# Kernel optimization log

Measured on AMD Instinct MI355X. Metric: run time of the kernel, lower is better.

## Reference

```python
import jax, jax.numpy as jnp
import numpy as np

N = 100000   # active voxels
C = 64       # inplanes
K3 = 27      # kernel^dim = 3^3 rulebook offsets
EPS = 1e-4   # scn.BatchNormReLU default eps


def setup_inputs() -> dict:
    key = jax.random.key(0)
    ks = jax.random.split(key, 14)
    features = jax.random.normal(ks[0], (N, C), dtype=jnp.float32)
    raw = jax.random.randint(ks[1], (N, K3), 0, 2 * N)
    neighbor_idx = jnp.where(raw < N, raw, -1).astype(jnp.int32)
    # center offset of a submanifold conv is always the site itself
    neighbor_idx = neighbor_idx.at[:, K3 // 2].set(jnp.arange(N, dtype=jnp.int32))

    def bn_params(k1, k2, k3, k4):
        gamma = 1.0 + 0.1 * jax.random.normal(k1, (C,), dtype=jnp.float32)
        beta = 0.1 * jax.random.normal(k2, (C,), dtype=jnp.float32)
        mean = 0.05 * jax.random.normal(k3, (C,), dtype=jnp.float32)
        var = 1.0 + 0.1 * jax.random.uniform(k4, (C,), dtype=jnp.float32)
        return gamma, beta, mean, var

    g1, b1, m1, v1 = bn_params(ks[2], ks[3], ks[4], ks[5])
    g2, b2, m2, v2 = bn_params(ks[6], ks[7], ks[8], ks[9])
    scale = 1.0 / np.sqrt(K3 * C)
    W1 = scale * jax.random.normal(ks[10], (K3, C, C), dtype=jnp.float32)
    W2 = scale * jax.random.normal(ks[11], (K3, C, C), dtype=jnp.float32)
    return {
        "features": features, "neighbor_idx": neighbor_idx,
        "gamma1": g1, "beta1": b1, "mean1": m1, "var1": v1, "W1": W1,
        "gamma2": g2, "beta2": b2, "mean2": m2, "var2": v2, "W2": W2,
    }


def _bn_relu(x, gamma, beta, mean, var):
    # eval-mode BatchNorm fused with ReLU, per channel
    return jax.nn.relu((x - mean) * jax.lax.rsqrt(var + EPS) * gamma + beta)


def _subm_conv(x, neighbor_idx, W):
    # gather neighbor features per rulebook offset, masked sum of per-offset GEMMs
    valid = neighbor_idx >= 0                       # [N, K3]
    g = x[jnp.where(valid, neighbor_idx, 0)]        # [N, K3, C]
    g = jnp.where(valid[..., None], g, 0.0)
    return jnp.einsum('nkc,kcd->nd', g, W)          # [N, C]


def reference(features, neighbor_idx, gamma1, beta1, mean1, var1, W1,
              gamma2, beta2, mean2, var2, W2):
    y = _bn_relu(features, gamma1, beta1, mean1, var1)
    y = _subm_conv(y, neighbor_idx, W1)
    y = _bn_relu(y, gamma2, beta2, mean2, var2)
    y = _subm_conv(y, neighbor_idx, W2)
    return features + y
```

## Files before the change

kernel.cpp:

```cpp
#include <hip/hip_runtime.h>
#include <hip/hip_bf16.h>

#define NS 100000
#define CC 64
#define K3 27
#define EPSV 1e-4f
#define NBLK 3125
#define PACKB 108

typedef __attribute__((ext_vector_type(4))) float f32x4;
typedef __attribute__((ext_vector_type(8))) short bf16x8;

__device__ __forceinline__ short f2bf(float f) {
    union { float f; unsigned u; } uf; uf.f = f;
    unsigned r = (uf.u + 0x7fffu + ((uf.u >> 16) & 1u)) >> 16;
    return (short)r;
}

__global__ __launch_bounds__(256) void prepare(
    const float* __restrict__ x,
    const float* __restrict__ g1, const float* __restrict__ b1,
    const float* __restrict__ m1, const float* __restrict__ v1,
    const float* __restrict__ W1, const float* __restrict__ W2,
    short* __restrict__ X1, short* __restrict__ X2,
    short* __restrict__ Wp1, short* __restrict__ Wp2)
{
    int blk = blockIdx.x;
    if (blk < NBLK) {
        int tid = blk * 256 + threadIdx.x;
        int ch8 = (tid & 7) * 8;
        float4 ga = *(const float4*)(g1 + ch8), gb = *(const float4*)(g1 + ch8 + 4);
        float4 ba = *(const float4*)(b1 + ch8), bb = *(const float4*)(b1 + ch8 + 4);
        float4 ma = *(const float4*)(m1 + ch8), mb = *(const float4*)(m1 + ch8 + 4);
        float4 va = *(const float4*)(v1 + ch8), vb = *(const float4*)(v1 + ch8 + 4);
        float g[8] = {ga.x,ga.y,ga.z,ga.w,gb.x,gb.y,gb.z,gb.w};
        float b[8] = {ba.x,ba.y,ba.z,ba.w,bb.x,bb.y,bb.z,bb.w};
        float m[8] = {ma.x,ma.y,ma.z,ma.w,mb.x,mb.y,mb.z,mb.w};
        float vv[8] = {va.x,va.y,va.z,va.w,vb.x,vb.y,vb.z,vb.w};
        const float* px = x + (long)tid * 8;
        float4 u = *(const float4*)px;
        float4 w = *(const float4*)(px + 4);
        float o[8] = {u.x,u.y,u.z,u.w,w.x,w.y,w.z,w.w};
        bf16x8 r;
#pragma unroll
        for (int j = 0; j < 8; ++j) {
            float s = g[j] * rsqrtf(vv[j] + EPSV);
            float bi = b[j] - m[j] * s;
            r[j] = f2bf(fmaxf(fmaf(o[j], s, bi), 0.f));
        }
        *(bf16x8*)(X1 + (long)tid * 8) = r;
        if (blk == 0 && threadIdx.x < 64) {
            X1[(long)NS * 64 + threadIdx.x] = 0;
            X2[(long)NS * 64 + threadIdx.x] = 0;
        }
    } else {
        int t = (blk - NBLK) * 256 + threadIdx.x;
        if (t >= 2 * K3 * 8 * 64) return;
        int lane = t & 63;
        int f = t >> 6;
        int which = f / (K3 * 8);
        int f2 = f % (K3 * 8);
        int k = f2 >> 3, kc = (f2 >> 2) & 1, t4 = f2 & 3;
        const float* W = which ? W2 : W1;
        short* Wp = which ? Wp2 : Wp1;
        int col = t4 * 16 + (lane & 15);
        int kr0 = kc * 32 + 8 * (lane >> 4);
        bf16x8 v;
#pragma unroll
        for (int j = 0; j < 8; ++j) v[j] = f2bf(W[(k * CC + kr0 + j) * CC + col]);
        *(bf16x8*)(Wp + ((long)f2 * 64 + lane) * 8) = v;
    }
}

template <int PHASE>
__global__ __launch_bounds__(256, 4) void subm_conv(
    const short* __restrict__ Xg,
    const int* __restrict__ nb,
    const short* __restrict__ Wp,
    const float* __restrict__ g2, const float* __restrict__ b2,
    const float* __restrict__ m2, const float* __restrict__ v2,
    const float* __restrict__ feat,
    short* __restrict__ Xout, float* __restrict__ yout)
{
    __shared__ float red[4][32][64];
    __shared__ float s2c[64], b2c[64];
    int lane = threadIdx.x & 63;
    int w = threadIdx.x >> 6;
    int base = blockIdx.x * 32;
    int r15 = lane & 15, hi = lane >> 4;
    int site0 = base + r15, site1 = base + 16 + r15;

    if (PHASE == 1 && threadIdx.x < 64) {
        float s = g2[threadIdx.x] * rsqrtf(v2[threadIdx.x] + EPSV);
        s2c[threadIdx.x] = s;
        b2c[threadIdx.x] = b2[threadIdx.x] - m2[threadIdx.x] * s;
    }

    int q0[7], q1[7];
#pragma unroll
    for (int j = 0; j < 7; ++j) {
        int k = w + 4 * j;
        int i0 = (k < K3) ? nb[site0 * K3 + k] : -1;
        int i1 = (k < K3) ? nb[site1 * K3 + k] : -1;
        q0[j] = (i0 < 0) ? NS : i0;
        q1[j] = (i1 < 0) ? NS : i1;
    }

    f32x4 acc[2][4] = {};
    const bf16x8* wpv = (const bf16x8*)Wp;
#pragma unroll
    for (int j = 0; j < 7; ++j) {
        int k = w + 4 * j;
        int kk = (k < K3) ? k : 0;
        const short* p0 = Xg + (long)q0[j] * 64 + hi * 8;
        const short* p1 = Xg + (long)q1[j] * 64 + hi * 8;
        bf16x8 a00 = *(const bf16x8*)p0;
        bf16x8 a01 = *(const bf16x8*)(p0 + 32);
        bf16x8 a10 = *(const bf16x8*)p1;
        bf16x8 a11 = *(const bf16x8*)(p1 + 32);
        const bf16x8* bp = wpv + (long)kk * 8 * 64 + lane;
#pragma unroll
        for (int t4 = 0; t4 < 4; ++t4) {
            bf16x8 b0 = bp[t4 * 64];
            bf16x8 b1 = bp[(4 + t4) * 64];
            acc[0][t4] = __builtin_amdgcn_mfma_f32_16x16x32_bf16(a00, b0, acc[0][t4], 0, 0, 0);
            acc[1][t4] = __builtin_amdgcn_mfma_f32_16x16x32_bf16(a10, b0, acc[1][t4], 0, 0, 0);
            acc[0][t4] = __builtin_amdgcn_mfma_f32_16x16x32_bf16(a01, b1, acc[0][t4], 0, 0, 0);
            acc[1][t4] = __builtin_amdgcn_mfma_f32_16x16x32_bf16(a11, b1, acc[1][t4], 0, 0, 0);
        }
    }

#pragma unroll
    for (int mt = 0; mt < 2; ++mt)
#pragma unroll
        for (int t4 = 0; t4 < 4; ++t4)
#pragma unroll
            for (int r = 0; r < 4; ++r)
                red[w][mt * 16 + hi * 4 + r][t4 * 16 + r15] = acc[mt][t4][r];
    __syncthreads();

    int t = threadIdx.x;
    int lr = t >> 3, c0 = (t & 7) * 8;
    int row = base + lr;
    float s[8];
#pragma unroll
    for (int c = 0; c < 8; ++c)
        s[c] = red[0][lr][c0 + c] + red[1][lr][c0 + c] +
               red[2][lr][c0 + c] + red[3][lr][c0 + c];
    if (PHASE == 1) {
        bf16x8 o;
#pragma unroll
        for (int c = 0; c < 8; ++c)
            o[c] = f2bf(fmaxf(fmaf(s[c], s2c[c0 + c], b2c[c0 + c]), 0.f));
        *(bf16x8*)(Xout + (long)row * 64 + c0) = o;
    } else {
        const float* fp = feat + (long)row * 64 + c0;
        float4 f0 = *(const float4*)fp, f1 = *(const float4*)(fp + 4);
        float4 o0 = {s[0] + f0.x, s[1] + f0.y, s[2] + f0.z, s[3] + f0.w};
        float4 o1 = {s[4] + f1.x, s[5] + f1.y, s[6] + f1.z, s[7] + f1.w};
        float* op = yout + (long)row * 64 + c0;
        *(float4*)op = o0;
        *(float4*)(op + 4) = o1;
    }
}

extern "C" void kernel_launch(void* const* d_in, const int* in_sizes, int n_in,
                              void* d_out, int out_size, void* d_ws, size_t ws_size,
                              hipStream_t stream) {
    const float* feat = (const float*)d_in[0];
    const int*   nb   = (const int*)d_in[1];
    const float* g1 = (const float*)d_in[2];
    const float* b1 = (const float*)d_in[3];
    const float* m1 = (const float*)d_in[4];
    const float* v1 = (const float*)d_in[5];
    const float* W1 = (const float*)d_in[6];
    const float* g2 = (const float*)d_in[7];
    const float* b2 = (const float*)d_in[8];
    const float* m2 = (const float*)d_in[9];
    const float* v2 = (const float*)d_in[10];
    const float* W2 = (const float*)d_in[11];
    float* out = (float*)d_out;

    char* ws = (char*)d_ws;
    short* X1 = (short*)ws;
    short* X2 = (short*)(ws + 12802048);
    short* Wp1 = (short*)(ws + 25604096);
    short* Wp2 = (short*)(ws + 25604096 + 221184);

    prepare<<<NBLK + PACKB, 256, 0, stream>>>(feat, g1, b1, m1, v1, W1, W2,
                                              X1, X2, Wp1, Wp2);
    subm_conv<1><<<NBLK, 256, 0, stream>>>(X1, nb, Wp1, g2, b2, m2, v2,
                                           nullptr, X2, nullptr);
    subm_conv<2><<<NBLK, 256, 0, stream>>>(X2, nb, Wp2, g2, b2, m2, v2,
                                           feat, nullptr, out);
}
```

Measured before the change: 227.0 us.

## Halve sites per block and skip gathers for missing neighbors

Each conv block now handles 16 sites instead of 32, doubling the grid and halving per-wave accumulators and LDS reduction space. Missing neighbors no longer load a zero row; the load is predicated off and zeros are used instead, saving gather traffic for the roughly half of offsets that are absent. In exchange, weight fragments are reloaded twice as often per site, each wave does half the MFMA work per weight load, and the output stores become narrower.

```diff
diff --git a/kernel.cpp b/kernel.cpp
--- a/kernel.cpp
+++ b/kernel.cpp
@@ -7,9 +7,11 @@
 #define EPSV 1e-4f
 #define NBLK 3125
 #define PACKB 108
+#define CBLK 6250
 
 typedef __attribute__((ext_vector_type(4))) float f32x4;
 typedef __attribute__((ext_vector_type(8))) short bf16x8;
+typedef __attribute__((ext_vector_type(4))) short s16x4;
 
 __device__ __forceinline__ short f2bf(float f) {
     union { float f; unsigned u; } uf; uf.f = f;
@@ -82,13 +84,13 @@
     const float* __restrict__ feat,
     short* __restrict__ Xout, float* __restrict__ yout)
 {
-    __shared__ float red[4][32][64];
+    __shared__ float red[4][16][64];
     __shared__ float s2c[64], b2c[64];
     int lane = threadIdx.x & 63;
     int w = threadIdx.x >> 6;
-    int base = blockIdx.x * 32;
+    int base = blockIdx.x * 16;
     int r15 = lane & 15, hi = lane >> 4;
-    int site0 = base + r15, site1 = base + 16 + r15;
+    int site = base + r15;
 
     if (PHASE == 1 && threadIdx.x < 64) {
         float s = g2[threadIdx.x] * rsqrtf(v2[threadIdx.x] + EPSV);
@@ -96,71 +98,61 @@
         b2c[threadIdx.x] = b2[threadIdx.x] - m2[threadIdx.x] * s;
     }
 
-    int q0[7], q1[7];
+    int q[7];
 #pragma unroll
     for (int j = 0; j < 7; ++j) {
         int k = w + 4 * j;
-        int i0 = (k < K3) ? nb[site0 * K3 + k] : -1;
-        int i1 = (k < K3) ? nb[site1 * K3 + k] : -1;
-        q0[j] = (i0 < 0) ? NS : i0;
-        q1[j] = (i1 < 0) ? NS : i1;
+        q[j] = (k < K3) ? nb[site * K3 + k] : -1;
     }
 
-    f32x4 acc[2][4] = {};
+    f32x4 acc[4] = {};
     const bf16x8* wpv = (const bf16x8*)Wp;
 #pragma unroll
     for (int j = 0; j < 7; ++j) {
         int k = w + 4 * j;
         int kk = (k < K3) ? k : 0;
-        const short* p0 = Xg + (long)q0[j] * 64 + hi * 8;
-        const short* p1 = Xg + (long)q1[j] * 64 + hi * 8;
-        bf16x8 a00 = *(const bf16x8*)p0;
-        bf16x8 a01 = *(const bf16x8*)(p0 + 32);
-        bf16x8 a10 = *(const bf16x8*)p1;
-        bf16x8 a11 = *(const bf16x8*)(p1 + 32);
+        bf16x8 a0 = {}, a1 = {};
+        if (q[j] >= 0) {
+            const short* p = Xg + (long)q[j] * 64 + hi * 8;
+            a0 = *(const bf16x8*)p;
+            a1 = *(const bf16x8*)(p + 32);
+        }
         const bf16x8* bp = wpv + (long)kk * 8 * 64 + lane;
 #pragma unroll
         for (int t4 = 0; t4 < 4; ++t4) {
             bf16x8 b0 = bp[t4 * 64];
             bf16x8 b1 = bp[(4 + t4) * 64];
-            acc[0][t4] = __builtin_amdgcn_mfma_f32_16x16x32_bf16(a00, b0, acc[0][t4], 0, 0, 0);
-            acc[1][t4] = __builtin_amdgcn_mfma_f32_16x16x32_bf16(a10, b0, acc[1][t4], 0, 0, 0);
-            acc[0][t4] = __builtin_amdgcn_mfma_f32_16x16x32_bf16(a01, b1, acc[0][t4], 0, 0, 0);
-            acc[1][t4] = __builtin_amdgcn_mfma_f32_16x16x32_bf16(a11, b1, acc[1][t4], 0, 0, 0);
+            acc[t4] = __builtin_amdgcn_mfma_f32_16x16x32_bf16(a0, b0, acc[t4], 0, 0, 0);
+            acc[t4] = __builtin_amdgcn_mfma_f32_16x16x32_bf16(a1, b1, acc[t4], 0, 0, 0);
         }
     }
 
 #pragma unroll
-    for (int mt = 0; mt < 2; ++mt)
+    for (int t4 = 0; t4 < 4; ++t4)
 #pragma unroll
-        for (int t4 = 0; t4 < 4; ++t4)
-#pragma unroll
-            for (int r = 0; r < 4; ++r)
-                red[w][mt * 16 + hi * 4 + r][t4 * 16 + r15] = acc[mt][t4][r];
+        for (int r = 0; r < 4; ++r)
+            red[w][hi * 4 + r][t4 * 16 + r15] = acc[t4][r];
     __syncthreads();
 
     int t = threadIdx.x;
-    int lr = t >> 3, c0 = (t & 7) * 8;
+    int lr = t >> 4, c0 = (t & 15) * 4;
     int row = base + lr;
-    float s[8];
+    float s[4];
 #pragma unroll
-    for (int c = 0; c < 8; ++c)
+    for (int c = 0; c < 4; ++c)
         s[c] = red[0][lr][c0 + c] + red[1][lr][c0 + c] +
                red[2][lr][c0 + c] + red[3][lr][c0 + c];
     if (PHASE == 1) {
-        bf16x8 o;
+        s16x4 o;
 #pragma unroll
-        for (int c = 0; c < 8; ++c)
+        for (int c = 0; c < 4; ++c)
             o[c] = f2bf(fmaxf(fmaf(s[c], s2c[c0 + c], b2c[c0 + c]), 0.f));
-        *(bf16x8*)(Xout + (long)row * 64 + c0) = o;
+        *(s16x4*)(Xout + (long)row * 64 + c0) = o;
     } else {
         const float* fp = feat + (long)row * 64 + c0;
-        float4 f0 = *(const float4*)fp, f1 = *(const float4*)(fp + 4);
+        float4 f0 = *(const float4*)fp;
         float4 o0 = {s[0] + f0.x, s[1] + f0.y, s[2] + f0.z, s[3] + f0.w};
-        float4 o1 = {s[4] + f1.x, s[5] + f1.y, s[6] + f1.z, s[7] + f1.w};
-        float* op = yout + (long)row * 64 + c0;
-        *(float4*)op = o0;
-        *(float4*)(op + 4) = o1;
+        *(float4*)(yout + (long)row * 64 + c0) = o0;
     }
 }
 
@@ -189,8 +181,8 @@
 
     prepare<<<NBLK + PACKB, 256, 0, stream>>>(feat, g1, b1, m1, v1, W1, W2,
                                               X1, X2, Wp1, Wp2);
-    subm_conv<1><<<NBLK, 256, 0, stream>>>(X1, nb, Wp1, g2, b2, m2, v2,
+    subm_conv<1><<<CBLK, 256, 0, stream>>>(X1, nb, Wp1, g2, b2, m2, v2,
                                            nullptr, X2, nullptr);
-    subm_conv<2><<<NBLK, 256, 0, stream>>>(X2, nb, Wp2, g2, b2, m2, v2,
+    subm_conv<2><<<CBLK, 256, 0, stream>>>(X2, nb, Wp2, g2, b2, m2, v2,
                                            feat, nullptr, out);
 }
```

Result: slower. 253.4 us (+11.6%).
